# Kernel optimization log

Measured on AMD Instinct MI355X. Metric: run time of the kernel, lower is better.

Reference implementation:

```python
import jax, jax.numpy as jnp
import numpy as np

D_MODEL = 1024
NUM_HEADS = 16
D_K = D_MODEL // NUM_HEADS


def setup_inputs() -> dict:
    key = jax.random.key(0)
    ks = jax.random.split(key, 5)
    x = jax.random.normal(ks[0], (8, 1024, D_MODEL), dtype=jnp.float32)
    s_in = 1.0 / np.sqrt(D_MODEL)
    W_qkv = jax.random.normal(ks[1], (D_MODEL, 3 * D_MODEL), dtype=jnp.float32) * s_in
    b_qkv = jax.random.normal(ks[2], (3 * D_MODEL,), dtype=jnp.float32) * 0.01
    W_o = jax.random.normal(ks[3], (D_MODEL, D_MODEL), dtype=jnp.float32) * s_in
    b_o = jax.random.normal(ks[4], (D_MODEL,), dtype=jnp.float32) * 0.01
    return {"x": x, "W_qkv": W_qkv, "b_qkv": b_qkv, "W_o": W_o, "b_o": b_o}


def reference(x, W_qkv, b_qkv, W_o, b_o):
    B, N, D = x.shape
    qkv = x @ W_qkv + b_qkv                      # [B, N, 3D]
    qkv = qkv.reshape(B, N, 3, NUM_HEADS, D_K)
    qkv = jnp.transpose(qkv, (2, 0, 3, 1, 4))    # [3, B, H, N, d_k]
    q, k, v = qkv[0], qkv[1], qkv[2]
    scale = 1.0 / np.sqrt(D_K).astype(np.float32)
    attn = jnp.einsum('bhqd,bhkd->bhqk', q, k) * scale
    attn = jax.nn.softmax(attn, axis=-1)
    out = jnp.einsum('bhqk,bhkd->bhqd', attn, v)  # [B, H, N, d_k]
    out = jnp.transpose(out, (0, 2, 1, 3)).reshape(B, N, D)
    return out @ W_o + b_o
```

## Files before the change

kernel.cpp:

```cpp
#include <hip/hip_runtime.h>


typedef __attribute__((ext_vector_type(8))) short bf16x8;
typedef __attribute__((ext_vector_type(4))) float f32x4;

#define GLOAD_LDS16(gp, lp)                                                              \
  __builtin_amdgcn_global_load_lds((const __attribute__((address_space(1))) void*)(gp),  \
                                   (__attribute__((address_space(3))) void*)(lp), 16, 0, 0)

__device__ __forceinline__ unsigned short f2bf(float f) {
  unsigned int u = __float_as_uint(f);
  u += 0x7fffu + ((u >> 16) & 1u);
  return (unsigned short)(u >> 16);
}

__global__ __launch_bounds__(256) void cast_f32_to_bf16(
    const float* __restrict__ in, unsigned short* __restrict__ out, int n4) {
  int stride = gridDim.x * blockDim.x;
  for (int i = blockIdx.x * blockDim.x + threadIdx.x; i < n4; i += stride) {
    float4 v = reinterpret_cast<const float4*>(in)[i];
    ushort4 o;
    o.x = f2bf(v.x); o.y = f2bf(v.y); o.z = f2bf(v.z); o.w = f2bf(v.w);
    reinterpret_cast<ushort4*>(out)[i] = o;
  }
}

__global__ __launch_bounds__(256) void transpose_cast(
    const float* __restrict__ W, unsigned short* __restrict__ Wt, int R, int C) {
  __shared__ float tile[32][33];
  int tx = threadIdx.x & 31, ty = threadIdx.x >> 5;
  int c0 = blockIdx.x * 32, r0 = blockIdx.y * 32;
  #pragma unroll
  for (int i = 0; i < 4; i++) {
    int r = r0 + ty + i * 8;
    tile[ty + i * 8][tx] = W[(size_t)r * C + c0 + tx];
  }
  __syncthreads();
  #pragma unroll
  for (int i = 0; i < 4; i++) {
    int c = c0 + ty + i * 8;
    Wt[(size_t)c * R + r0 + tx] = f2bf(tile[tx][ty + i * 8]);
  }
}

template <int MODE>
__global__ __launch_bounds__(512) void gemm256(
    const unsigned short* __restrict__ A, const unsigned short* __restrict__ Bt,
    const float* __restrict__ bias, unsigned short* __restrict__ qkv_out,
    float* __restrict__ Cout) {
  __shared__ __align__(16) unsigned short As[3][128 * 64];
  __shared__ __align__(16) unsigned short Bs[3][256 * 64];
  const int t = threadIdx.x;
  const int lane = t & 63, wid = t >> 6;
  const int lr = lane & 15, g = lane >> 4;
  const int wm = wid >> 2, wn = wid & 3;

  const int nwg = gridDim.x * gridDim.y;
  const int id = blockIdx.x + gridDim.x * blockIdx.y;
  const int sw = (id & 7) * (nwg >> 3) + (id >> 3);
  const int bx = sw % gridDim.x, by = sw / gridDim.x;
  const int row0 = by * 128, col0 = bx * 256;

  const int srow = t >> 3, sch = t & 7;

  auto stA = [&](int buf, int kt, int j) {
    int row = j * 64 + srow;
    int ch = sch ^ (row & 7);
    GLOAD_LDS16(A + (size_t)(row0 + row) * 1024 + kt * 64 + ch * 8,
                (char*)&As[buf][0] + j * 8192 + t * 16);
  };
  auto stB = [&](int buf, int kt, int j) {
    int row = j * 64 + srow;
    int ch = sch ^ (row & 7);
    GLOAD_LDS16(Bt + (size_t)(col0 + row) * 1024 + kt * 64 + ch * 8,
                (char*)&Bs[buf][0] + j * 8192 + t * 16);
  };
  auto rdA = [&](int buf, int c, int m) -> bf16x8 {
    int r = wm * 64 + m * 16 + lr;
    return *(const bf16x8*)((const char*)&As[buf][0] + r * 128 +
                            ((c * 64 + g * 16) ^ ((r & 7) << 4)));
  };
  auto rdB = [&](int buf, int c, int n) -> bf16x8 {
    int r = wn * 64 + n * 16 + lr;
    return *(const bf16x8*)((const char*)&Bs[buf][0] + r * 128 +
                            ((c * 64 + g * 16) ^ ((r & 7) << 4)));
  };

  f32x4 acc[4][4] = {};

  stA(0, 0, 0); stA(0, 0, 1);
  stB(0, 0, 0); stB(0, 0, 1); stB(0, 0, 2); stB(0, 0, 3);
  stA(1, 1, 0); stA(1, 1, 1);
  stB(1, 1, 0); stB(1, 1, 1); stB(1, 1, 2); stB(1, 1, 3);
  asm volatile("s_waitcnt vmcnt(6)" ::: "memory");
  __builtin_amdgcn_s_barrier();

  for (int kt = 0; kt < 16; kt++) {
    const int buf = kt % 3;
    const int bufn = (kt + 2) % 3;
    const bool pf = (kt <= 13);
    if (kt > 0) {
      if (kt == 15) asm volatile("s_waitcnt vmcnt(0)" ::: "memory");
      else          asm volatile("s_waitcnt vmcnt(6)" ::: "memory");
      __builtin_amdgcn_s_barrier();
    }

    bf16x8 a0[4], b0[4];
    #pragma unroll
    for (int m = 0; m < 4; m++) a0[m] = rdA(buf, 0, m);
    #pragma unroll
    for (int n = 0; n < 4; n++) b0[n] = rdB(buf, 0, n);
    if (pf) { stA(bufn, kt + 2, 0); stA(bufn, kt + 2, 1); stB(bufn, kt + 2, 0); }
    __builtin_amdgcn_s_barrier();
    asm volatile("s_waitcnt lgkmcnt(0)" ::: "memory");
    __builtin_amdgcn_sched_barrier(0);
    __builtin_amdgcn_s_setprio(1);
    #pragma unroll
    for (int m = 0; m < 4; m++)
      #pragma unroll
      for (int n = 0; n < 4; n++)
        acc[m][n] = __builtin_amdgcn_mfma_f32_16x16x32_bf16(a0[m], b0[n], acc[m][n], 0, 0, 0);
    __builtin_amdgcn_s_setprio(0);
    __builtin_amdgcn_s_barrier();

    bf16x8 a1[4], b1[4];
    #pragma unroll
    for (int m = 0; m < 4; m++) a1[m] = rdA(buf, 1, m);
    #pragma unroll
    for (int n = 0; n < 4; n++) b1[n] = rdB(buf, 1, n);
    if (pf) { stB(bufn, kt + 2, 1); stB(bufn, kt + 2, 2); stB(bufn, kt + 2, 3); }
    __builtin_amdgcn_s_barrier();
    asm volatile("s_waitcnt lgkmcnt(0)" ::: "memory");
    __builtin_amdgcn_sched_barrier(0);
    __builtin_amdgcn_s_setprio(1);
    #pragma unroll
    for (int m = 0; m < 4; m++)
      #pragma unroll
      for (int n = 0; n < 4; n++)
        acc[m][n] = __builtin_amdgcn_mfma_f32_16x16x32_bf16(a1[m], b1[n], acc[m][n], 0, 0, 0);
    __builtin_amdgcn_s_setprio(0);
    __builtin_amdgcn_s_barrier();
  }

  if (MODE == 0) {
    const int which = col0 >> 10;
    if (which == 2) {
      #pragma unroll
      for (int m = 0; m < 4; m++) {
        int row = row0 + wm * 64 + m * 16 + g * 4;
        int bb = row >> 10, nn = row & 1023;
        #pragma unroll
        for (int n = 0; n < 4; n++) {
          int col = col0 + wn * 64 + n * 16 + lr;
          int cc = col & 1023;
          int h = cc >> 6, dk = cc & 63;
          float bv = bias[col];
          ushort4 w;
          w.x = f2bf(acc[m][n][0] + bv);
          w.y = f2bf(acc[m][n][1] + bv);
          w.z = f2bf(acc[m][n][2] + bv);
          w.w = f2bf(acc[m][n][3] + bv);
          size_t idx = ((size_t)2 << 23) + (((size_t)(bb * 16 + h)) << 16) +
                       (size_t)dk * 1024 + nn;
          *(ushort4*)(qkv_out + idx) = w;
        }
      }
    } else {
      #pragma unroll
      for (int m = 0; m < 4; m++) {
        #pragma unroll
        for (int n = 0; n < 4; n++) {
          int col = col0 + wn * 64 + n * 16 + lr;
          int cc = col & 1023;
          int h = cc >> 6, dk = cc & 63;
          #pragma unroll
          for (int r = 0; r < 4; r++) {
            int row = row0 + wm * 64 + m * 16 + g * 4 + r;
            int bb = row >> 10, nn = row & 1023;
            float v = acc[m][n][r] + bias[col];
            if (which == 0) v *= 0.125f;
            size_t idx = ((size_t)which << 23) +
                         (((size_t)((bb * 16 + h) * 1024 + nn)) << 6) + dk;
            qkv_out[idx] = f2bf(v);
          }
        }
      }
    }
  } else {
    #pragma unroll
    for (int m = 0; m < 4; m++) {
      #pragma unroll
      for (int n = 0; n < 4; n++) {
        int col = col0 + wn * 64 + n * 16 + lr;
        #pragma unroll
        for (int r = 0; r < 4; r++) {
          int row = row0 + wm * 64 + m * 16 + g * 4 + r;
          Cout[(size_t)row * 1024 + col] = acc[m][n][r] + bias[col];
        }
      }
    }
  }
}

__global__ __launch_bounds__(512) void attn_mfma(
    const unsigned short* __restrict__ qkv, unsigned short* __restrict__ attn_out) {
  __shared__ __align__(16) unsigned short K_lds[2][64 * 64];
  __shared__ __align__(16) unsigned short V_lds[2][64 * 64];
  __shared__ __align__(16) unsigned short P_lds[128 * 64];

  const int bid = ((blockIdx.x & 7) << 7) + (blockIdx.x >> 3);
  const int bh = bid >> 3, qt = bid & 7;
  const unsigned short* Qp = qkv + ((size_t)bh << 16);
  const unsigned short* Kp = qkv + (1u << 23) + ((size_t)bh << 16);
  const unsigned short* Vt = qkv + (2u << 23) + ((size_t)bh << 16);

  const int t = threadIdx.x;
  const int lane = t & 63, wid = t >> 6;
  const int lr = lane & 15, g = lane >> 4;

  bf16x8 qf[2];
  {
    int qrow = qt * 128 + wid * 16 + lr;
    qf[0] = *(const bf16x8*)(Qp + (size_t)qrow * 64 + g * 8);
    qf[1] = *(const bf16x8*)(Qp + (size_t)qrow * 64 + 32 + g * 8);
  }

  const int srow = t >> 3;
  const int sch  = (t & 7) ^ (srow & 7);
  const int so   = t * 16;

  auto stage = [&](int buf, int kt) {
    GLOAD_LDS16(Kp + (size_t)(kt * 64 + srow) * 64 + sch * 8, (char*)&K_lds[buf][0] + so);
    GLOAD_LDS16(Vt + (size_t)srow * 1024 + kt * 64 + sch * 8, (char*)&V_lds[buf][0] + so);
  };

  f32x4 o_acc[4] = {};
  float den[4] = {0.f, 0.f, 0.f, 0.f};

  stage(0, 0);
  __syncthreads();
  int buf = 0;
  for (int kt = 0; kt < 16; kt++) {
    if (kt + 1 < 16) stage(buf ^ 1, kt + 1);

    f32x4 s4[4] = {};
    __builtin_amdgcn_s_setprio(1);
    #pragma unroll
    for (int ks = 0; ks < 4; ks++) {
      int krow = ks * 16 + lr;
      #pragma unroll
      for (int c = 0; c < 2; c++) {
        bf16x8 kf = *(const bf16x8*)((char*)&K_lds[buf][0] + krow * 128 +
                                     ((c * 64 + g * 16) ^ ((krow & 7) << 4)));
        s4[ks] = __builtin_amdgcn_mfma_f32_16x16x32_bf16(qf[c], kf, s4[ks], 0, 0, 0);
      }
    }
    __builtin_amdgcn_s_setprio(0);

    #pragma unroll
    for (int ks = 0; ks < 4; ks++) {
      #pragma unroll
      for (int r = 0; r < 4; r++) {
        float e = __expf(s4[ks][r]);
        den[r] += e;
        int q = wid * 16 + g * 4 + r;
        *(unsigned short*)((char*)P_lds + q * 128 +
                           (((ks * 16 + lr) * 2) ^ ((q & 7) << 4))) = f2bf(e);
      }
    }

    bf16x8 pa[2];
    {
      int q = wid * 16 + lr;
      #pragma unroll
      for (int c = 0; c < 2; c++)
        pa[c] = *(const bf16x8*)((char*)P_lds + q * 128 +
                                 ((c * 64 + g * 16) ^ ((q & 7) << 4)));
    }
    __builtin_amdgcn_s_setprio(1);
    #pragma unroll
    for (int ds_ = 0; ds_ < 4; ds_++) {
      int drow = ds_ * 16 + lr;
      #pragma unroll
      for (int c = 0; c < 2; c++) {
        bf16x8 vf = *(const bf16x8*)((char*)&V_lds[buf][0] + drow * 128 +
                                     ((c * 64 + g * 16) ^ ((drow & 7) << 4)));
        o_acc[ds_] = __builtin_amdgcn_mfma_f32_16x16x32_bf16(pa[c], vf, o_acc[ds_], 0, 0, 0);
      }
    }
    __builtin_amdgcn_s_setprio(0);
    __syncthreads();
    buf ^= 1;
  }

  #pragma unroll
  for (int r = 0; r < 4; r++) {
    den[r] += __shfl_xor(den[r], 1, 64);
    den[r] += __shfl_xor(den[r], 2, 64);
    den[r] += __shfl_xor(den[r], 4, 64);
    den[r] += __shfl_xor(den[r], 8, 64);
  }

  const int bb = bh >> 4, h = bh & 15;
  #pragma unroll
  for (int ds_ = 0; ds_ < 4; ds_++) {
    #pragma unroll
    for (int r = 0; r < 4; r++) {
      int q = qt * 128 + wid * 16 + g * 4 + r;
      int d = h * 64 + ds_ * 16 + lr;
      attn_out[((size_t)(bb * 1024 + q)) * 1024 + d] = f2bf(o_acc[ds_][r] / den[r]);
    }
  }
}

extern "C" void kernel_launch(void* const* d_in, const int* in_sizes, int n_in,
                              void* d_out, int out_size, void* d_ws, size_t ws_size,
                              hipStream_t stream) {
  const float* x     = (const float*)d_in[0];
  const float* W_qkv = (const float*)d_in[1];
  const float* b_qkv = (const float*)d_in[2];
  const float* W_o   = (const float*)d_in[3];
  const float* b_o   = (const float*)d_in[4];
  float* out = (float*)d_out;

  unsigned short* ws      = (unsigned short*)d_ws;
  unsigned short* x_bf    = ws;
  unsigned short* wqkv_t  = x_bf + 8388608;
  unsigned short* wo_t    = wqkv_t + 3145728;
  unsigned short* qkv     = wo_t + 1048576;
  unsigned short* attn_o  = qkv + 25165824;

  cast_f32_to_bf16<<<2048, 256, 0, stream>>>(x, x_bf, 8388608 / 4);
  transpose_cast<<<dim3(96, 32), 256, 0, stream>>>(W_qkv, wqkv_t, 1024, 3072);
  transpose_cast<<<dim3(32, 32), 256, 0, stream>>>(W_o, wo_t, 1024, 1024);

  gemm256<0><<<dim3(12, 64), 512, 0, stream>>>(x_bf, wqkv_t, b_qkv, qkv, nullptr);
  attn_mfma<<<1024, 512, 0, stream>>>(qkv, attn_o);
  gemm256<1><<<dim3(4, 64), 512, 0, stream>>>(attn_o, wo_t, b_o, nullptr, out);
}
```

Measured before the change: 159.8 us.

## Use 256x256 tiles with 4-stage BK=32 pipeline for QKV projection GEMM

Splits the templated GEMM into a dedicated QKV kernel and an output-projection kernel. The QKV kernel now uses 256x256 output tiles with a 32-wide K step, a 4-deep global-to-LDS pipeline, an XOR swizzle for the narrower rows, and launch bounds requesting 2 blocks per CU. Each wave computes its output in two halves so A loads interleave with MFMA work. The goal is more reuse of each loaded A/B tile and deeper prefetch, at the cost of higher register pressure (8x4 accumulators) and fewer blocks (384) to spread across CUs.

```diff
diff --git a/kernel.cpp b/kernel.cpp
--- a/kernel.cpp
+++ b/kernel.cpp
@@ -43,11 +43,128 @@
   }
 }
 
-template <int MODE>
-__global__ __launch_bounds__(512) void gemm256(
+__global__ __launch_bounds__(512, 2) void gemm1_k(
     const unsigned short* __restrict__ A, const unsigned short* __restrict__ Bt,
-    const float* __restrict__ bias, unsigned short* __restrict__ qkv_out,
-    float* __restrict__ Cout) {
+    const float* __restrict__ bias, unsigned short* __restrict__ qkv_out) {
+  __shared__ __align__(16) unsigned short As[4][256 * 32];
+  __shared__ __align__(16) unsigned short Bs[4][256 * 32];
+
+  const int t = threadIdx.x;
+  const int lane = t & 63, wid = t >> 6;
+  const int lr = lane & 15, g = lane >> 4;
+  const int wm = wid >> 2, wn = wid & 3;
+
+  const int nwg = gridDim.x * gridDim.y;
+  const int id = blockIdx.x + gridDim.x * blockIdx.y;
+  const int sw = (id & 7) * (nwg >> 3) + (id >> 3);
+  const int bx = sw % gridDim.x, by = sw / gridDim.x;
+  const int row0 = by * 256, col0 = bx * 256;
+
+  const int srow = t >> 2;
+  const int sch  = (t & 3) ^ ((srow >> 1) & 3);
+
+  auto stA = [&](int buf, int kt, int j) {
+    GLOAD_LDS16(A + (size_t)(row0 + j * 128 + srow) * 1024 + kt * 32 + sch * 8,
+                (char*)&As[buf][0] + j * 8192 + t * 16);
+  };
+  auto stB = [&](int buf, int kt, int j) {
+    GLOAD_LDS16(Bt + (size_t)(col0 + j * 128 + srow) * 1024 + kt * 32 + sch * 8,
+                (char*)&Bs[buf][0] + j * 8192 + t * 16);
+  };
+  auto rdA = [&](int buf, int m) -> bf16x8 {
+    int r = wm * 128 + m * 16 + lr;
+    return *(const bf16x8*)((const char*)&As[buf][0] + r * 64 +
+                            ((g ^ ((r >> 1) & 3)) * 16));
+  };
+  auto rdB = [&](int buf, int n) -> bf16x8 {
+    int r = wn * 64 + n * 16 + lr;
+    return *(const bf16x8*)((const char*)&Bs[buf][0] + r * 64 +
+                            ((g ^ ((r >> 1) & 3)) * 16));
+  };
+
+  f32x4 acc[8][4] = {};
+
+  stA(0, 0, 0); stA(0, 0, 1); stB(0, 0, 0); stB(0, 0, 1);
+  stA(1, 1, 0); stA(1, 1, 1); stB(1, 1, 0); stB(1, 1, 1);
+  stA(2, 2, 0); stA(2, 2, 1); stB(2, 2, 0); stB(2, 2, 1);
+
+  for (int kt = 0; kt < 32; kt++) {
+    const int buf = kt & 3;
+    if (kt <= 29)      asm volatile("s_waitcnt vmcnt(8)" ::: "memory");
+    else if (kt == 30) asm volatile("s_waitcnt vmcnt(4)" ::: "memory");
+    else               asm volatile("s_waitcnt vmcnt(0)" ::: "memory");
+    __builtin_amdgcn_s_barrier();
+
+    bf16x8 bfr[4], afr[4];
+
+    #pragma unroll
+    for (int n = 0; n < 4; n++) bfr[n] = rdB(buf, n);
+    #pragma unroll
+    for (int m = 0; m < 4; m++) afr[m] = rdA(buf, m);
+    if (kt <= 28) { stA((kt + 3) & 3, kt + 3, 0); stA((kt + 3) & 3, kt + 3, 1); }
+    __builtin_amdgcn_s_barrier();
+    asm volatile("s_waitcnt lgkmcnt(0)" ::: "memory");
+    __builtin_amdgcn_sched_barrier(0);
+    __builtin_amdgcn_s_setprio(1);
+    #pragma unroll
+    for (int m = 0; m < 4; m++)
+      #pragma unroll
+      for (int n = 0; n < 4; n++)
+        acc[m][n] = __builtin_amdgcn_mfma_f32_16x16x32_bf16(afr[m], bfr[n], acc[m][n], 0, 0, 0);
+    __builtin_amdgcn_s_setprio(0);
+
+    #pragma unroll
+    for (int m = 0; m < 4; m++) afr[m] = rdA(buf, 4 + m);
+    if (kt <= 28) { stB((kt + 3) & 3, kt + 3, 0); stB((kt + 3) & 3, kt + 3, 1); }
+    __builtin_amdgcn_s_barrier();
+    asm volatile("s_waitcnt lgkmcnt(0)" ::: "memory");
+    __builtin_amdgcn_sched_barrier(0);
+    __builtin_amdgcn_s_setprio(1);
+    #pragma unroll
+    for (int m = 0; m < 4; m++)
+      #pragma unroll
+      for (int n = 0; n < 4; n++)
+        acc[4 + m][n] = __builtin_amdgcn_mfma_f32_16x16x32_bf16(afr[m], bfr[n], acc[4 + m][n], 0, 0, 0);
+    __builtin_amdgcn_s_setprio(0);
+    __builtin_amdgcn_s_barrier();
+  }
+
+  const int which = col0 >> 10;
+  #pragma unroll
+  for (int m = 0; m < 8; m++) {
+    const int row = row0 + wm * 128 + m * 16 + g * 4;
+    const int bb = row >> 10, nn = row & 1023;
+    #pragma unroll
+    for (int n = 0; n < 4; n++) {
+      const int col = col0 + wn * 64 + n * 16 + lr;
+      const int cc = col & 1023;
+      const int h = cc >> 6, dk = cc & 63;
+      const float bv = bias[col];
+      if (which == 2) {
+        ushort4 w;
+        w.x = f2bf(acc[m][n][0] + bv);
+        w.y = f2bf(acc[m][n][1] + bv);
+        w.z = f2bf(acc[m][n][2] + bv);
+        w.w = f2bf(acc[m][n][3] + bv);
+        size_t idx = ((size_t)2 << 23) + (((size_t)(bb * 16 + h)) << 16) +
+                     (size_t)dk * 1024 + nn;
+        *(ushort4*)(qkv_out + idx) = w;
+      } else {
+        const float sc = (which == 0) ? 0.125f : 1.0f;
+        #pragma unroll
+        for (int r = 0; r < 4; r++) {
+          size_t idx = ((size_t)which << 23) +
+                       (((size_t)((bb * 16 + h) * 1024 + nn + r)) << 6) + dk;
+          qkv_out[idx] = f2bf((acc[m][n][r] + bv) * sc);
+        }
+      }
+    }
+  }
+}
+
+__global__ __launch_bounds__(512) void gemm2_k(
+    const unsigned short* __restrict__ A, const unsigned short* __restrict__ Bt,
+    const float* __restrict__ bias, float* __restrict__ Cout) {
   __shared__ __align__(16) unsigned short As[3][128 * 64];
   __shared__ __align__(16) unsigned short Bs[3][256 * 64];
   const int t = threadIdx.x;
@@ -142,61 +259,15 @@
     __builtin_amdgcn_s_barrier();
   }
 
-  if (MODE == 0) {
-    const int which = col0 >> 10;
-    if (which == 2) {
-      #pragma unroll
-      for (int m = 0; m < 4; m++) {
-        int row = row0 + wm * 64 + m * 16 + g * 4;
-        int bb = row >> 10, nn = row & 1023;
-        #pragma unroll
-        for (int n = 0; n < 4; n++) {
-          int col = col0 + wn * 64 + n * 16 + lr;
-          int cc = col & 1023;
-          int h = cc >> 6, dk = cc & 63;
-          float bv = bias[col];
-          ushort4 w;
-          w.x = f2bf(acc[m][n][0] + bv);
-          w.y = f2bf(acc[m][n][1] + bv);
-          w.z = f2bf(acc[m][n][2] + bv);
-          w.w = f2bf(acc[m][n][3] + bv);
-          size_t idx = ((size_t)2 << 23) + (((size_t)(bb * 16 + h)) << 16) +
-                       (size_t)dk * 1024 + nn;
-          *(ushort4*)(qkv_out + idx) = w;
-        }
-      }
-    } else {
-      #pragma unroll
-      for (int m = 0; m < 4; m++) {
-        #pragma unroll
-        for (int n = 0; n < 4; n++) {
-          int col = col0 + wn * 64 + n * 16 + lr;
-          int cc = col & 1023;
-          int h = cc >> 6, dk = cc & 63;
-          #pragma unroll
-          for (int r = 0; r < 4; r++) {
-            int row = row0 + wm * 64 + m * 16 + g * 4 + r;
-            int bb = row >> 10, nn = row & 1023;
-            float v = acc[m][n][r] + bias[col];
-            if (which == 0) v *= 0.125f;
-            size_t idx = ((size_t)which << 23) +
-                         (((size_t)((bb * 16 + h) * 1024 + nn)) << 6) + dk;
-            qkv_out[idx] = f2bf(v);
-          }
-        }
-      }
-    }
-  } else {
-    #pragma unroll
-    for (int m = 0; m < 4; m++) {
-      #pragma unroll
-      for (int n = 0; n < 4; n++) {
-        int col = col0 + wn * 64 + n * 16 + lr;
-        #pragma unroll
-        for (int r = 0; r < 4; r++) {
-          int row = row0 + wm * 64 + m * 16 + g * 4 + r;
-          Cout[(size_t)row * 1024 + col] = acc[m][n][r] + bias[col];
-        }
+  #pragma unroll
+  for (int m = 0; m < 4; m++) {
+    #pragma unroll
+    for (int n = 0; n < 4; n++) {
+      int col = col0 + wn * 64 + n * 16 + lr;
+      #pragma unroll
+      for (int r = 0; r < 4; r++) {
+        int row = row0 + wm * 64 + m * 16 + g * 4 + r;
+        Cout[(size_t)row * 1024 + col] = acc[m][n][r] + bias[col];
       }
     }
   }
@@ -334,7 +405,7 @@
   transpose_cast<<<dim3(96, 32), 256, 0, stream>>>(W_qkv, wqkv_t, 1024, 3072);
   transpose_cast<<<dim3(32, 32), 256, 0, stream>>>(W_o, wo_t, 1024, 1024);
 
-  gemm256<0><<<dim3(12, 64), 512, 0, stream>>>(x_bf, wqkv_t, b_qkv, qkv, nullptr);
+  gemm1_k<<<dim3(12, 32), 512, 0, stream>>>(x_bf, wqkv_t, b_qkv, qkv);
   attn_mfma<<<1024, 512, 0, stream>>>(qkv, attn_o);
-  gemm256<1><<<dim3(4, 64), 512, 0, stream>>>(attn_o, wo_t, b_o, nullptr, out);
-}
+  gemm2_k<<<dim3(4, 64), 512, 0, stream>>>(attn_o, wo_t, b_o, out);
+}
```

After: 169.8 us. +6.3%, slower.

## Fuse prep kernels and load V fragments directly from global in attention

Applied to the files above, without the earlier changes.

Merges the x cast and the two weight transpose-casts into one kernel launch, split by block index, to cut launch overhead. In the attention kernel, V is no longer staged through double-buffered LDS. Each wave loads its V MFMA fragments straight from global memory into registers every iteration. This reduces LDS usage and LDS traffic, but exposes global load latency that is not prefetched ahead of use.

```diff
diff --git a/kernel.cpp b/kernel.cpp
--- a/kernel.cpp
+++ b/kernel.cpp
@@ -14,32 +14,44 @@
   return (unsigned short)(u >> 16);
 }
 
-__global__ __launch_bounds__(256) void cast_f32_to_bf16(
-    const float* __restrict__ in, unsigned short* __restrict__ out, int n4) {
-  int stride = gridDim.x * blockDim.x;
-  for (int i = blockIdx.x * blockDim.x + threadIdx.x; i < n4; i += stride) {
-    float4 v = reinterpret_cast<const float4*>(in)[i];
-    ushort4 o;
-    o.x = f2bf(v.x); o.y = f2bf(v.y); o.z = f2bf(v.z); o.w = f2bf(v.w);
-    reinterpret_cast<ushort4*>(out)[i] = o;
-  }
-}
-
-__global__ __launch_bounds__(256) void transpose_cast(
-    const float* __restrict__ W, unsigned short* __restrict__ Wt, int R, int C) {
-  __shared__ float tile[32][33];
-  int tx = threadIdx.x & 31, ty = threadIdx.x >> 5;
-  int c0 = blockIdx.x * 32, r0 = blockIdx.y * 32;
-  #pragma unroll
-  for (int i = 0; i < 4; i++) {
-    int r = r0 + ty + i * 8;
-    tile[ty + i * 8][tx] = W[(size_t)r * C + c0 + tx];
-  }
-  __syncthreads();
-  #pragma unroll
-  for (int i = 0; i < 4; i++) {
-    int c = c0 + ty + i * 8;
-    Wt[(size_t)c * R + r0 + tx] = f2bf(tile[tx][ty + i * 8]);
+__global__ __launch_bounds__(256) void prep_fused(
+    const float* __restrict__ x, unsigned short* __restrict__ x_bf,
+    const float* __restrict__ W_qkv, unsigned short* __restrict__ wqkv_t,
+    const float* __restrict__ W_o, unsigned short* __restrict__ wo_t) {
+  const int b = blockIdx.x;
+  if (b < 2048) {
+    const int n4 = 8388608 / 4;
+    for (int i = b * 256 + threadIdx.x; i < n4; i += 2048 * 256) {
+      float4 v = reinterpret_cast<const float4*>(x)[i];
+      ushort4 o;
+      o.x = f2bf(v.x); o.y = f2bf(v.y); o.z = f2bf(v.z); o.w = f2bf(v.w);
+      reinterpret_cast<ushort4*>(x_bf)[i] = o;
+    }
+  } else {
+    __shared__ float tile[32][33];
+    const float* W;
+    unsigned short* Wt;
+    int R = 1024, C, bx, by;
+    if (b < 5120) {
+      W = W_qkv; Wt = wqkv_t; C = 3072;
+      int bb = b - 2048; bx = bb % 96; by = bb / 96;
+    } else {
+      W = W_o; Wt = wo_t; C = 1024;
+      int bb = b - 5120; bx = bb & 31; by = bb >> 5;
+    }
+    const int tx = threadIdx.x & 31, ty = threadIdx.x >> 5;
+    const int c0 = bx * 32, r0 = by * 32;
+    #pragma unroll
+    for (int i = 0; i < 4; i++) {
+      int r = r0 + ty + i * 8;
+      tile[ty + i * 8][tx] = W[(size_t)r * C + c0 + tx];
+    }
+    __syncthreads();
+    #pragma unroll
+    for (int i = 0; i < 4; i++) {
+      int c = c0 + ty + i * 8;
+      Wt[(size_t)c * R + r0 + tx] = f2bf(tile[tx][ty + i * 8]);
+    }
   }
 }
 
@@ -205,7 +217,6 @@
 __global__ __launch_bounds__(512) void attn_mfma(
     const unsigned short* __restrict__ qkv, unsigned short* __restrict__ attn_out) {
   __shared__ __align__(16) unsigned short K_lds[2][64 * 64];
-  __shared__ __align__(16) unsigned short V_lds[2][64 * 64];
   __shared__ __align__(16) unsigned short P_lds[128 * 64];
 
   const int bid = ((blockIdx.x & 7) << 7) + (blockIdx.x >> 3);
@@ -229,19 +240,18 @@
   const int sch  = (t & 7) ^ (srow & 7);
   const int so   = t * 16;
 
-  auto stage = [&](int buf, int kt) {
+  auto stageK = [&](int buf, int kt) {
     GLOAD_LDS16(Kp + (size_t)(kt * 64 + srow) * 64 + sch * 8, (char*)&K_lds[buf][0] + so);
-    GLOAD_LDS16(Vt + (size_t)srow * 1024 + kt * 64 + sch * 8, (char*)&V_lds[buf][0] + so);
   };
 
   f32x4 o_acc[4] = {};
   float den[4] = {0.f, 0.f, 0.f, 0.f};
 
-  stage(0, 0);
+  stageK(0, 0);
   __syncthreads();
   int buf = 0;
   for (int kt = 0; kt < 16; kt++) {
-    if (kt + 1 < 16) stage(buf ^ 1, kt + 1);
+    if (kt + 1 < 16) stageK(buf ^ 1, kt + 1);
 
     f32x4 s4[4] = {};
     __builtin_amdgcn_s_setprio(1);
@@ -256,6 +266,14 @@
       }
     }
     __builtin_amdgcn_s_setprio(0);
+
+    bf16x8 vfr[4][2];
+    #pragma unroll
+    for (int ds_ = 0; ds_ < 4; ds_++)
+      #pragma unroll
+      for (int c = 0; c < 2; c++)
+        vfr[ds_][c] = *(const bf16x8*)(Vt + (size_t)(ds_ * 16 + lr) * 1024 +
+                                       kt * 64 + c * 32 + g * 8);
 
     #pragma unroll
     for (int ks = 0; ks < 4; ks++) {
@@ -279,15 +297,10 @@
     }
     __builtin_amdgcn_s_setprio(1);
     #pragma unroll
-    for (int ds_ = 0; ds_ < 4; ds_++) {
-      int drow = ds_ * 16 + lr;
-      #pragma unroll
-      for (int c = 0; c < 2; c++) {
-        bf16x8 vf = *(const bf16x8*)((char*)&V_lds[buf][0] + drow * 128 +
-                                     ((c * 64 + g * 16) ^ ((drow & 7) << 4)));
-        o_acc[ds_] = __builtin_amdgcn_mfma_f32_16x16x32_bf16(pa[c], vf, o_acc[ds_], 0, 0, 0);
-      }
-    }
+    for (int ds_ = 0; ds_ < 4; ds_++)
+      #pragma unroll
+      for (int c = 0; c < 2; c++)
+        o_acc[ds_] = __builtin_amdgcn_mfma_f32_16x16x32_bf16(pa[c], vfr[ds_][c], o_acc[ds_], 0, 0, 0);
     __builtin_amdgcn_s_setprio(0);
     __syncthreads();
     buf ^= 1;
@@ -330,10 +343,7 @@
   unsigned short* qkv     = wo_t + 1048576;
   unsigned short* attn_o  = qkv + 25165824;
 
-  cast_f32_to_bf16<<<2048, 256, 0, stream>>>(x, x_bf, 8388608 / 4);
-  transpose_cast<<<dim3(96, 32), 256, 0, stream>>>(W_qkv, wqkv_t, 1024, 3072);
-  transpose_cast<<<dim3(32, 32), 256, 0, stream>>>(W_o, wo_t, 1024, 1024);
-
+  prep_fused<<<6144, 256, 0, stream>>>(x, x_bf, W_qkv, wqkv_t, W_o, wo_t);
   gemm256<0><<<dim3(12, 64), 512, 0, stream>>>(x_bf, wqkv_t, b_qkv, qkv, nullptr);
   attn_mfma<<<1024, 512, 0, stream>>>(qkv, attn_o);
   gemm256<1><<<dim3(4, 64), 512, 0, stream>>>(attn_o, wo_t, b_o, nullptr, out);
```

Result: slower. 235.3 us (+47.2%).
